# Kernel tuning notes

Hardware: AMD Instinct MI355X
Metric: run time of the kernel (lower is better)

The kernel has to match this reference:

```python
import jax, jax.numpy as jnp
import numpy as np

EMBED_DIM = 1024
NUM_HEADS = 16
HEAD_DIM = EMBED_DIM // NUM_HEADS


def setup_inputs() -> dict:
    key = jax.random.key(0)
    ks = jax.random.split(key, 9)
    s = 1.0 / np.sqrt(EMBED_DIM)
    X = jax.random.normal(ks[0], (4, 2048, EMBED_DIM), dtype=jnp.float32)
    # Linear weights stored as [in, out] for x @ W + b
    Wq = jax.random.uniform(ks[1], (EMBED_DIM, EMBED_DIM), jnp.float32, -s, s)
    bq = jax.random.uniform(ks[2], (EMBED_DIM,), jnp.float32, -s, s)
    Wk = jax.random.uniform(ks[3], (EMBED_DIM, EMBED_DIM), jnp.float32, -s, s)
    bk = jax.random.uniform(ks[4], (EMBED_DIM,), jnp.float32, -s, s)
    Wv = jax.random.uniform(ks[5], (EMBED_DIM, EMBED_DIM), jnp.float32, -s, s)
    bv = jax.random.uniform(ks[6], (EMBED_DIM,), jnp.float32, -s, s)
    Wo = jax.random.uniform(ks[7], (EMBED_DIM, EMBED_DIM), jnp.float32, -s, s)
    bo = jax.random.uniform(ks[8], (EMBED_DIM,), jnp.float32, -s, s)
    return {"X": X, "Wq": Wq, "bq": bq, "Wk": Wk, "bk": bk,
            "Wv": Wv, "bv": bv, "Wo": Wo, "bo": bo}


def reference(X, Wq, bq, Wk, bk, Wv, bv, Wo, bo):
    B, S, _ = X.shape
    def split_heads(t):  # [B,S,E] -> [B,H,S,D]
        return t.reshape(B, S, NUM_HEADS, HEAD_DIM).transpose(0, 2, 1, 3)
    Q = split_heads(X @ Wq + bq)
    K = split_heads(X @ Wk + bk)
    V = split_heads(X @ Wv + bv)
    scale = 1.0 / np.sqrt(HEAD_DIM).astype(np.float32)
    scores = jnp.einsum('bhqd,bhkd->bhqk', Q, K) * scale
    probs = jax.nn.softmax(scores, axis=-1)
    attn = jnp.einsum('bhqk,bhkd->bhqd', probs, V)  # [B,H,S,D]
    combined = attn.transpose(0, 2, 1, 3).reshape(B, S, EMBED_DIM)
    return combined @ Wo + bo
```

## Files before the change

kernel.cpp:

```cpp
#include <hip/hip_runtime.h>
#include <hip/hip_bf16.h>

#define EMBED 1024
#define NHEADS 16
#define HDIM 64
#define SEQ 2048
#define BATCH 4
#define ROWS (BATCH * SEQ)

typedef __attribute__((ext_vector_type(8))) short bf16x8;
typedef __attribute__((ext_vector_type(4))) float f32x4;
typedef __attribute__((ext_vector_type(2))) float f32x2;
typedef __attribute__((ext_vector_type(16))) float f32x16;
typedef __attribute__((ext_vector_type(4))) unsigned int u32x4;
typedef __attribute__((ext_vector_type(2))) unsigned int u32x2;
typedef __attribute__((ext_vector_type(2))) int i32x2;
typedef unsigned int u32;

#define SL2E 0.18033688011112042f

__device__ __forceinline__ short f2bf(float f) {
    u32 u = __builtin_bit_cast(u32, f) + 0x8000u;
    return (short)(u >> 16);
}

__device__ __forceinline__ u32 pkbf(float a, float b) {
    u32 ua = __builtin_bit_cast(u32, a) + 0x8000u;
    u32 ub = __builtin_bit_cast(u32, b) + 0x8000u;
    return __builtin_amdgcn_perm(ua, ub, 0x03020706u);
}

__device__ __forceinline__ u32 cvtpk(float a, float b) {
    u32 r;
    asm("v_cvt_pk_bf16_f32 %0, %1, %2" : "=v"(r) : "v"(a), "v"(b));
    return r;
}

__device__ __forceinline__ float fexp2(float x) {
#if __has_builtin(__builtin_amdgcn_exp2f)
    return __builtin_amdgcn_exp2f(x);
#else
    return exp2f(x);
#endif
}

__device__ __forceinline__ void async16(const void* g, void* l) {
    __builtin_amdgcn_global_load_lds((const __attribute__((address_space(1))) u32*)g,
                                     (__attribute__((address_space(3))) u32*)l, 16, 0, 0);
}

__global__ __launch_bounds__(256) void prep(const float* __restrict__ X,
                                            short* __restrict__ Xbf,
                                            const float* __restrict__ W0,
                                            const float* __restrict__ W1,
                                            const float* __restrict__ W2,
                                            const float* __restrict__ W3,
                                            short* __restrict__ T0,
                                            short* __restrict__ T1,
                                            short* __restrict__ T2,
                                            short* __restrict__ T3) {
    const int bid = blockIdx.x;
    if (bid < 8192) {
        int i = (bid * 256 + threadIdx.x) * 4;
        float4 v = *(const float4*)&X[i];
        u32x2 o = { pkbf(v.x, v.y), pkbf(v.z, v.w) };
        *(u32x2*)&Xbf[i] = o;
        return;
    }
    const int id = bid - 8192;
    const int z = id >> 8;
    const int rem = id & 255;
    const int n0 = (rem & 15) * 64, k0 = (rem >> 4) * 64;
    const float* W = (z == 0) ? W0 : (z == 1) ? W1 : (z == 2) ? W2 : W3;
    short* WT = (z == 0) ? T0 : (z == 1) ? T1 : (z == 2) ? T2 : T3;
    const float sc = (z == 0) ? SL2E : 1.0f;
    __shared__ float T[64][65];
    const int rr = threadIdx.x >> 4, cc = (threadIdx.x & 15) * 4;
    #pragma unroll
    for (int p = 0; p < 4; ++p) {
        int r = p * 16 + rr;
        float4 v = *(const float4*)&W[(size_t)(k0 + r) * EMBED + n0 + cc];
        T[r][cc] = v.x * sc; T[r][cc + 1] = v.y * sc; T[r][cc + 2] = v.z * sc; T[r][cc + 3] = v.w * sc;
    }
    __syncthreads();
    #pragma unroll
    for (int p = 0; p < 4; ++p) {
        int r = p * 16 + rr;
        u32x2 o = { pkbf(T[cc][r], T[cc + 1][r]), pkbf(T[cc + 2][r], T[cc + 3][r]) };
        *(u32x2*)&WT[(size_t)(n0 + r) * EMBED + k0 + cc] = o;
    }
}

__global__ __launch_bounds__(512, 2) void gemm_p128(const short* __restrict__ A,
                                                    const short* __restrict__ BT,
                                                    const float* __restrict__ b0,
                                                    const float* __restrict__ b1,
                                                    const float* __restrict__ b2,
                                                    void* __restrict__ C0,
                                                    void* __restrict__ C1,
                                                    void* __restrict__ C2,
                                                    int mode) {
    __shared__ short As[2][8192];
    __shared__ short Bs[2][16384];
    const int tid = threadIdx.x;
    const int lane = tid & 63;
    const int wid = tid >> 6;
    const int c16 = lane & 15, quad = lane >> 4, sw = c16 & 7;
    const int wm = wid >> 2, wn = wid & 3;
    const int gx = gridDim.x;
    const int hid = blockIdx.y * gx + blockIdx.x;
    const int cpx = (gx * gridDim.y) >> 3;
    const int tle = (hid & 7) * cpx + (hid >> 3);
    const int bx = tle % gx, by = tle / gx;
    const int rowblk = by * 128, colblk = bx * 256;

    const int r0 = tid >> 3;
    const int g0 = (tid & 7) ^ (r0 & 7);
    const short* aS0 = A + (size_t)(rowblk + r0) * EMBED + g0 * 8;
    const short* bS0 = BT + (size_t)(colblk + r0) * EMBED + g0 * 8;

#define STAGE_A(SBUF, V) do { \
    const short* _s = aS0 + (V) * 64; \
    async16(_s,         &As[SBUF][tid * 8]); \
    async16(_s + 65536, &As[SBUF][tid * 8 + 4096]); \
} while (0)
#define STAGE_B0(SBUF, V) do { \
    const short* _s = bS0 + (V) * 64; \
    async16(_s,         &Bs[SBUF][tid * 8]); \
    async16(_s + 65536, &Bs[SBUF][tid * 8 + 4096]); \
} while (0)
#define STAGE_B1(SBUF, V) do { \
    const short* _s = bS0 + 131072 + (V) * 64; \
    async16(_s,         &Bs[SBUF][tid * 8 + 8192]); \
    async16(_s + 65536, &Bs[SBUF][tid * 8 + 12288]); \
} while (0)

    f32x4 acc[4][4] = {};
    bf16x8 aU[2][2], bE[2][2], bO[2][2];

#define LDA(BUF, MH) do { \
    _Pragma("unroll") \
    for (int fm = 0; fm < 2; ++fm) { \
        const int row = wm * 64 + (MH) * 32 + fm * 16 + c16; \
        _Pragma("unroll") \
        for (int ks = 0; ks < 2; ++ks) \
            aU[fm][ks] = *(const bf16x8*)&As[BUF][row * 64 + ((ks * 4 + quad) ^ sw) * 8]; \
    } \
} while (0)
#define LDB(BUF, NH, DST) do { \
    _Pragma("unroll") \
    for (int fn = 0; fn < 2; ++fn) { \
        const int col = wn * 64 + (NH) * 32 + fn * 16 + c16; \
        _Pragma("unroll") \
        for (int ks = 0; ks < 2; ++ks) \
            DST[fn][ks] = *(const bf16x8*)&Bs[BUF][col * 64 + ((ks * 4 + quad) ^ sw) * 8]; \
    } \
} while (0)
#define MM(MB, NB, BM_) do { \
    _Pragma("unroll") \
    for (int fm = 0; fm < 2; ++fm) \
        _Pragma("unroll") \
        for (int fn = 0; fn < 2; ++fn) \
            _Pragma("unroll") \
            for (int ks = 0; ks < 2; ++ks) \
                acc[(MB) + fm][(NB) + fn] = \
                    __builtin_amdgcn_mfma_f32_16x16x32_bf16(aU[fm][ks], BM_[fn][ks], \
                        acc[(MB) + fm][(NB) + fn], 0, 0, 0); \
} while (0)
#define PH_MID() do { \
    __builtin_amdgcn_s_barrier(); \
    asm volatile("s_waitcnt lgkmcnt(0)" ::: "memory"); \
    __builtin_amdgcn_s_setprio(1); \
} while (0)
#define PH_END(VM) do { \
    __builtin_amdgcn_s_setprio(0); \
    if (VM) asm volatile("s_waitcnt vmcnt(6)" ::: "memory"); \
    __builtin_amdgcn_s_barrier(); \
} while (0)

    STAGE_B0(0, 0); STAGE_A(0, 0); STAGE_B1(0, 0);
    STAGE_B0(1, 1); STAGE_A(1, 1); STAGE_B1(1, 1);
    asm volatile("s_waitcnt vmcnt(6)" ::: "memory");
    __builtin_amdgcn_s_barrier();

    #pragma unroll 1
    for (int it = 0; it < 8; ++it) {
        const int u = 2 * it;
        const int v2 = (u + 2) & 15, v3 = (u + 3) & 15;
        LDA(0, 0); LDB(0, 0, bE);                     PH_MID(); MM(0, 0, bE); PH_END(0);
        LDB(0, 1, bO);            STAGE_B0(0, v2);    PH_MID(); MM(0, 2, bO); PH_END(0);
        LDA(0, 1);                STAGE_B1(0, v2);    PH_MID(); MM(2, 2, bO); PH_END(0);
                 STAGE_A(0, v2);     PH_MID(); MM(2, 0, bE); PH_END(1);
        LDA(1, 0); LDB(1, 0, bE);                     PH_MID(); MM(0, 0, bE); PH_END(0);
        LDB(1, 1, bO);            STAGE_B0(1, v3);    PH_MID(); MM(0, 2, bO); PH_END(0);
        LDA(1, 1);                STAGE_B1(1, v3);    PH_MID(); MM(2, 2, bO); PH_END(0);
                 STAGE_A(1, v3);     PH_MID(); MM(2, 0, bE); PH_END(1);
    }

    asm volatile("s_waitcnt vmcnt(0)" ::: "memory");

    const int rb0 = rowblk + wm * 64 + quad * 4;
    const int cb0 = wn * 64 + c16;
    if (mode == 0) {
        const int z = colblk >> 10;
        const int cm = colblk & 1023;
        const float* bias = (z == 0) ? b0 : (z == 1) ? b1 : b2;
        if (z == 2) {
            short* Vt = (short*)C2;
            #pragma unroll
            for (int m = 0; m < 4; ++m) {
                const int row = rb0 + (m >> 1) * 32 + (m & 1) * 16;
                const int b = row >> 11, s = row & 2047;
                #pragma unroll
                for (int n = 0; n < 4; ++n) {
                    const int cv = cm + cb0 + (n >> 1) * 32 + (n & 1) * 16;
                    const int head = cv >> 6, d = cv & 63;
                    const float bv = bias[cv];
                    u32x2 o = { pkbf(acc[m][n][0] + bv, acc[m][n][1] + bv),
                                pkbf(acc[m][n][2] + bv, acc[m][n][3] + bv) };
                    *(u32x2*)&Vt[((size_t)(b * NHEADS + head) * HDIM + d) * SEQ + s] = o;
                }
            }
        } else {
            short* Cq = (short*)((z == 0) ? C0 : C1);
            const float bsc = (z == 0) ? SL2E : 1.0f;
            #pragma unroll
            for (int m = 0; m < 4; ++m) {
                const int row = rb0 + (m >> 1) * 32 + (m & 1) * 16;
                #pragma unroll
                for (int n = 0; n < 4; ++n) {
                    const int col = cm + cb0 + (n >> 1) * 32 + (n & 1) * 16;
                    const float bv = bias[col] * bsc;
                    #pragma unroll
                    for (int r = 0; r < 4; ++r)
                        Cq[(size_t)(row + r) * EMBED + col] = f2bf(acc[m][n][r] + bv);
                }
            }
        }
    } else {
        float* Co = (float*)C0;
        #pragma unroll
        for (int m = 0; m < 4; ++m) {
            const int row = rb0 + (m >> 1) * 32 + (m & 1) * 16;
            #pragma unroll
            for (int n = 0; n < 4; ++n) {
                const int col = colblk + cb0 + (n >> 1) * 32 + (n & 1) * 16;
                const float bv = b0[col];
                #pragma unroll
                for (int r = 0; r < 4; ++r)
                    Co[(size_t)(row + r) * EMBED + col] = acc[m][n][r] + bv;
            }
        }
    }
#undef PH_END
#undef PH_MID
#undef MM
#undef LDB
#undef LDA
#undef STAGE_B1
#undef STAGE_B0
#undef STAGE_A
}

__global__ __launch_bounds__(512, 2) void gemm_k64(const short* __restrict__ A,
                                                   const short* __restrict__ BT,
                                                   const float* __restrict__ bias,
                                                   float* __restrict__ C) {
    __shared__ short As[2][8192];
    __shared__ short Bs[2][8192];
    const int tid = threadIdx.x;
    const int lane = tid & 63, wid = tid >> 6;
    const int c16 = lane & 15, quad = lane >> 4, sw = c16 & 7;
    const int wm = wid >> 2, wn = wid & 3;
    const int gx = gridDim.x;
    const int hid = blockIdx.y * gx + blockIdx.x;
    const int cpx = (gx * gridDim.y) >> 3;
    const int tle = (hid & 7) * cpx + (hid >> 3);
    const int bx = tle % gx, by = tle / gx;
    const int rowblk = by * 128, colblk = bx * 128;

    const int r0 = tid >> 3;
    const int g0 = (tid & 7) ^ (r0 & 7);
    const short* aS = A + (size_t)(rowblk + r0) * EMBED + g0 * 8;
    const short* bS = BT + (size_t)(colblk + r0) * EMBED + g0 * 8;

#define STG(SBUF, V) do { \
    const short* _a = aS + (V) * 64; \
    const short* _b = bS + (V) * 64; \
    async16(_a,         &As[SBUF][tid * 8]); \
    async16(_a + 65536, &As[SBUF][tid * 8 + 4096]); \
    async16(_b,         &Bs[SBUF][tid * 8]); \
    async16(_b + 65536, &Bs[SBUF][tid * 8 + 4096]); \
} while (0)

    f32x4 acc[4][2] = {};

    STG(0, 0);
    asm volatile("s_waitcnt vmcnt(0)" ::: "memory");
    __builtin_amdgcn_s_barrier();

    #pragma unroll 2
    for (int t = 0; t < 16; ++t) {
        const int cur = t & 1;
        if (t < 15) STG(cur ^ 1, t + 1);
        bf16x8 af[4][2], bfv[2][2];
        #pragma unroll
        for (int fm = 0; fm < 4; ++fm) {
            const int row = wm * 64 + fm * 16 + c16;
            #pragma unroll
            for (int ks = 0; ks < 2; ++ks)
                af[fm][ks] = *(const bf16x8*)&As[cur][row * 64 + ((ks * 4 + quad) ^ sw) * 8];
        }
        #pragma unroll
        for (int fn = 0; fn < 2; ++fn) {
            const int col = wn * 32 + fn * 16 + c16;
            #pragma unroll
            for (int ks = 0; ks < 2; ++ks)
                bfv[fn][ks] = *(const bf16x8*)&Bs[cur][col * 64 + ((ks * 4 + quad) ^ sw) * 8];
        }
        __builtin_amdgcn_s_setprio(1);
        #pragma unroll
        for (int fm = 0; fm < 4; ++fm)
            #pragma unroll
            for (int fn = 0; fn < 2; ++fn)
                #pragma unroll
                for (int ks = 0; ks < 2; ++ks)
                    acc[fm][fn] = __builtin_amdgcn_mfma_f32_16x16x32_bf16(af[fm][ks], bfv[fn][ks], acc[fm][fn], 0, 0, 0);
        __builtin_amdgcn_s_setprio(0);
        asm volatile("s_waitcnt vmcnt(0)" ::: "memory");
        __builtin_amdgcn_s_barrier();
    }

    const int rb0 = rowblk + wm * 64 + quad * 4;
    const int cb0 = colblk + wn * 32 + c16;
    #pragma unroll
    for (int fm = 0; fm < 4; ++fm) {
        const int row = rb0 + fm * 16;
        #pragma unroll
        for (int fn = 0; fn < 2; ++fn) {
            const int col = cb0 + fn * 16;
            const float bv = bias[col];
            #pragma unroll
            for (int r = 0; r < 4; ++r)
                C[(size_t)(row + r) * EMBED + col] = acc[fm][fn][r] + bv;
        }
    }
#undef STG
}

__global__ __launch_bounds__(256, 4) void attn_mfma(const short* __restrict__ Qb,
                                                    const short* __restrict__ Kb,
                                                    const short* __restrict__ Vt,
                                                    short* __restrict__ Ob) {
    __shared__ short SH[16384];
    const int tid = threadIdx.x;
    const int wave = tid >> 6, lane = tid & 63;
    const int l31 = lane & 31, h = lane >> 5;
    const int swz = l31 & 7;
    const int hid = blockIdx.y * 16 + blockIdx.x;
    const int tle = (hid & 7) * 128 + (hid >> 3);
    const int qb = tle & 15, bh = tle >> 4;
    const int b = bh >> 4, hd = bh & 15;
    const size_t base = (size_t)b * SEQ * EMBED + (size_t)hd * HDIM;
    const size_t vbase = (size_t)bh * HDIM * SEQ;
    const int q0 = qb * 128;

    bf16x8 qf[4];
    #pragma unroll
    for (int ks = 0; ks < 4; ++ks)
        qf[ks] = *(const bf16x8*)&Qb[base + (size_t)(q0 + wave * 32 + l31) * EMBED + ks * 16 + h * 8];

    const short* kp[2];
    const short* vp[2];
    int ldofs[2];
    #pragma unroll
    for (int it = 0; it < 2; ++it) {
        int ci = (it * 4 + wave) * 64 + lane;
        int row = ci >> 3, g = (ci & 7) ^ (row & 7);
        kp[it] = Kb + base + (size_t)row * EMBED + g * 8;
        vp[it] = Vt + vbase + (size_t)row * SEQ + g * 8;
        ldofs[it] = (it * 4 + wave) * 512;
    }

#define STAGE_KV(J) do { \
    async16(kp[0], &SH[(J) * 4096 + ldofs[0]]); \
    async16(kp[1], &SH[(J) * 4096 + ldofs[1]]); \
    async16(vp[0], &SH[8192 + (J) * 4096 + ldofs[0]]); \
    async16(vp[1], &SH[8192 + (J) * 4096 + ldofs[1]]); \
    kp[0] += 64 * EMBED; kp[1] += 64 * EMBED; \
    vp[0] += 64; vp[1] += 64; \
} while (0)

    f32x16 O[2] = {};
    f32x2 ls = {0.0f, 0.0f};

    STAGE_KV(0);
    asm volatile("s_waitcnt vmcnt(0)" ::: "memory");
    __builtin_amdgcn_s_barrier();

#define ATT_TILE(CUR, NXT, DO_STAGE) do { \
    if (DO_STAGE) STAGE_KV(NXT); \
    _Pragma("unroll") \
    for (int nt = 0; nt < 2; ++nt) { \
        f32x16 st = {0.0f, 0.0f, 0.0f, 0.0f, 0.0f, 0.0f, 0.0f, 0.0f, \
                     0.0f, 0.0f, 0.0f, 0.0f, 0.0f, 0.0f, 0.0f, 0.0f}; \
        __builtin_amdgcn_s_setprio(1); \
        _Pragma("unroll") \
        for (int ks = 0; ks < 4; ++ks) { \
            bf16x8 ak = *(const bf16x8*)&SH[(CUR) * 4096 + (nt * 32 + l31) * 64 + ((ks * 2 + h) ^ swz) * 8]; \
            st = __builtin_amdgcn_mfma_f32_32x32x16_bf16(ak, qf[ks], st, 0, 0, 0); \
        } \
        __builtin_amdgcn_s_setprio(0); \
        u32 pk[8]; \
        _Pragma("unroll") \
        for (int i = 0; i < 8; ++i) { \
            float e0 = fexp2(st[2 * i]), e1 = fexp2(st[2 * i + 1]); \
            f32x2 e = { e0, e1 }; \
            ls += e; \
            pk[i] = cvtpk(e0, e1); \
        } \
        __builtin_amdgcn_s_setprio(1); \
        _Pragma("unroll") \
        for (int kk = 0; kk < 2; ++kk) { \
            const int ks = nt * 2 + kk, bs = kk * 4; \
            u32x4 fr; \
            i32x2 sA = __builtin_amdgcn_permlane32_swap((int)pk[bs + 0], (int)pk[bs + 2], false, false); \
            i32x2 sB = __builtin_amdgcn_permlane32_swap((int)pk[bs + 1], (int)pk[bs + 3], false, false); \
            fr.x = (u32)sA.x; fr.y = (u32)sB.x; fr.z = (u32)sA.y; fr.w = (u32)sB.y; \
            bf16x8 pf = __builtin_bit_cast(bf16x8, fr); \
            _Pragma("unroll") \
            for (int mt = 0; mt < 2; ++mt) { \
                bf16x8 vf = *(const bf16x8*)&SH[8192 + (CUR) * 4096 + (mt * 32 + l31) * 64 + ((ks * 2 + h) ^ swz) * 8]; \
                O[mt] = __builtin_amdgcn_mfma_f32_32x32x16_bf16(vf, pf, O[mt], 0, 0, 0); \
            } \
        } \
        __builtin_amdgcn_s_setprio(0); \
    } \
    asm volatile("s_waitcnt vmcnt(0)" ::: "memory"); \
    __builtin_amdgcn_s_barrier(); \
} while (0)

    #pragma unroll 1
    for (int t = 0; t < 30; t += 2) {
        ATT_TILE(0, 1, 1);
        ATT_TILE(1, 0, 1);
    }
    ATT_TILE(0, 1, 1);
    ATT_TILE(1, 0, 0);

#undef ATT_TILE
#undef STAGE_KV

    float lsum = ls.x + ls.y;
    lsum += __shfl_xor(lsum, 32);
    float inv = 1.0f / lsum;

    const int wbase = wave * 2048;
    #pragma unroll
    for (int mt = 0; mt < 2; ++mt)
        #pragma unroll
        for (int m = 0; m < 4; ++m) {
            u32x2 wv;
            wv.x = pkbf(O[mt][4 * m + 0] * inv, O[mt][4 * m + 1] * inv);
            wv.y = pkbf(O[mt][4 * m + 2] * inv, O[mt][4 * m + 3] * inv);
            int u = mt * 8 + 2 * m + h;
            int su = u ^ ((l31 & 7) << 1);
            *(u32x2*)&SH[wbase + l31 * 64 + su * 4] = wv;
        }
    __syncthreads();
    #pragma unroll
    for (int p = 0; p < 4; ++p) {
        int ci = p * 256 + tid;
        int wq = ci >> 8, rem = ci & 255;
        int r = rem >> 3, cch = rem & 7;
        int su = (2 * cch) ^ ((r & 7) << 1);
        bf16x8 val = *(const bf16x8*)&SH[wq * 2048 + r * 64 + su * 4];
        *(bf16x8*)&Ob[base + (size_t)(q0 + wq * 32 + r) * EMBED + cch * 8] = val;
    }
}

extern "C" void kernel_launch(void* const* d_in, const int* in_sizes, int n_in,
                              void* d_out, int out_size, void* d_ws, size_t ws_size,
                              hipStream_t stream)
{
    const float* X  = (const float*)d_in[0];
    const float* Wq = (const float*)d_in[1];
    const float* bq = (const float*)d_in[2];
    const float* Wk = (const float*)d_in[3];
    const float* bk = (const float*)d_in[4];
    const float* Wv = (const float*)d_in[5];
    const float* bv = (const float*)d_in[6];
    const float* Wo = (const float*)d_in[7];
    const float* bo = (const float*)d_in[8];
    float* out = (float*)d_out;

    const size_t NE = (size_t)ROWS * EMBED;
    short* Xbf = (short*)d_ws;
    short* Qb  = Xbf + NE;
    short* Kb  = Qb + NE;
    short* Vtb = Kb + NE;
    short* WqT = Vtb + NE;
    short* WkT = WqT + (size_t)EMBED * EMBED;
    short* WvT = WkT + (size_t)EMBED * EMBED;
    short* WoT = WvT + (size_t)EMBED * EMBED;

    prep<<<9216, 256, 0, stream>>>(X, Xbf, Wq, Wk, Wv, Wo, WqT, WkT, WvT, WoT);

    dim3 gq(12, 64, 1);
    gemm_p128<<<gq, 512, 0, stream>>>(Xbf, WqT, bq, bk, bv, Qb, Kb, Vtb, 0);

    dim3 gt(SEQ / 128, BATCH * NHEADS);
    attn_mfma<<<gt, 256, 0, stream>>>(Qb, Kb, Vtb, Qb);

    dim3 gg(8, 64, 1);
    gemm_k64<<<gg, 512, 0, stream>>>(Qb, WoT, bo, out);
}
```

Measured before the change: 255.9 us.

## Replace 128x256 ping-pong QKV GEMM with simpler 128x128 double-buffered kernel

The QKV projection GEMM moves from a 128x256 tile with a phased ping-pong schedule (barriers, priority toggling, partial vmcnt waits) to a 128x128 tile with a plain double-buffered loop. It also launches twice as many blocks and halves the shared-memory B buffer. The aim is better occupancy, a simpler schedule and less barrier overhead. The trade-offs are lower arithmetic intensity per tile, more redundant A loads, and a full vmcnt(0) wait every K step, which removes the fine-grained overlap.

```diff
diff --git a/kernel.cpp b/kernel.cpp
--- a/kernel.cpp
+++ b/kernel.cpp
@@ -91,20 +91,18 @@
     }
 }
 
-__global__ __launch_bounds__(512, 2) void gemm_p128(const short* __restrict__ A,
-                                                    const short* __restrict__ BT,
-                                                    const float* __restrict__ b0,
-                                                    const float* __restrict__ b1,
-                                                    const float* __restrict__ b2,
-                                                    void* __restrict__ C0,
-                                                    void* __restrict__ C1,
-                                                    void* __restrict__ C2,
-                                                    int mode) {
+__global__ __launch_bounds__(512, 2) void gemm_qkv128(const short* __restrict__ A,
+                                                      const short* __restrict__ BT,
+                                                      const float* __restrict__ b0,
+                                                      const float* __restrict__ b1,
+                                                      const float* __restrict__ b2,
+                                                      short* __restrict__ Cq,
+                                                      short* __restrict__ Ck,
+                                                      short* __restrict__ Vt) {
     __shared__ short As[2][8192];
-    __shared__ short Bs[2][16384];
+    __shared__ short Bs[2][8192];
     const int tid = threadIdx.x;
-    const int lane = tid & 63;
-    const int wid = tid >> 6;
+    const int lane = tid & 63, wid = tid >> 6;
     const int c16 = lane & 15, quad = lane >> 4, sw = c16 & 7;
     const int wm = wid >> 2, wn = wid & 3;
     const int gx = gridDim.x;
@@ -112,154 +110,97 @@
     const int cpx = (gx * gridDim.y) >> 3;
     const int tle = (hid & 7) * cpx + (hid >> 3);
     const int bx = tle % gx, by = tle / gx;
-    const int rowblk = by * 128, colblk = bx * 256;
+    const int rowblk = by * 128, colblk = bx * 128;
 
     const int r0 = tid >> 3;
     const int g0 = (tid & 7) ^ (r0 & 7);
-    const short* aS0 = A + (size_t)(rowblk + r0) * EMBED + g0 * 8;
-    const short* bS0 = BT + (size_t)(colblk + r0) * EMBED + g0 * 8;
-
-#define STAGE_A(SBUF, V) do { \
-    const short* _s = aS0 + (V) * 64; \
-    async16(_s,         &As[SBUF][tid * 8]); \
-    async16(_s + 65536, &As[SBUF][tid * 8 + 4096]); \
+    const short* aS = A + (size_t)(rowblk + r0) * EMBED + g0 * 8;
+    const short* bS = BT + (size_t)(colblk + r0) * EMBED + g0 * 8;
+
+#define STG(SBUF, V) do { \
+    const short* _a = aS + (V) * 64; \
+    const short* _b = bS + (V) * 64; \
+    async16(_a,         &As[SBUF][tid * 8]); \
+    async16(_a + 65536, &As[SBUF][tid * 8 + 4096]); \
+    async16(_b,         &Bs[SBUF][tid * 8]); \
+    async16(_b + 65536, &Bs[SBUF][tid * 8 + 4096]); \
 } while (0)
-#define STAGE_B0(SBUF, V) do { \
-    const short* _s = bS0 + (V) * 64; \
-    async16(_s,         &Bs[SBUF][tid * 8]); \
-    async16(_s + 65536, &Bs[SBUF][tid * 8 + 4096]); \
-} while (0)
-#define STAGE_B1(SBUF, V) do { \
-    const short* _s = bS0 + 131072 + (V) * 64; \
-    async16(_s,         &Bs[SBUF][tid * 8 + 8192]); \
-    async16(_s + 65536, &Bs[SBUF][tid * 8 + 12288]); \
-} while (0)
-
-    f32x4 acc[4][4] = {};
-    bf16x8 aU[2][2], bE[2][2], bO[2][2];
-
-#define LDA(BUF, MH) do { \
-    _Pragma("unroll") \
-    for (int fm = 0; fm < 2; ++fm) { \
-        const int row = wm * 64 + (MH) * 32 + fm * 16 + c16; \
-        _Pragma("unroll") \
-        for (int ks = 0; ks < 2; ++ks) \
-            aU[fm][ks] = *(const bf16x8*)&As[BUF][row * 64 + ((ks * 4 + quad) ^ sw) * 8]; \
-    } \
-} while (0)
-#define LDB(BUF, NH, DST) do { \
-    _Pragma("unroll") \
-    for (int fn = 0; fn < 2; ++fn) { \
-        const int col = wn * 64 + (NH) * 32 + fn * 16 + c16; \
-        _Pragma("unroll") \
-        for (int ks = 0; ks < 2; ++ks) \
-            DST[fn][ks] = *(const bf16x8*)&Bs[BUF][col * 64 + ((ks * 4 + quad) ^ sw) * 8]; \
-    } \
-} while (0)
-#define MM(MB, NB, BM_) do { \
-    _Pragma("unroll") \
-    for (int fm = 0; fm < 2; ++fm) \
-        _Pragma("unroll") \
-        for (int fn = 0; fn < 2; ++fn) \
-            _Pragma("unroll") \
-            for (int ks = 0; ks < 2; ++ks) \
-                acc[(MB) + fm][(NB) + fn] = \
-                    __builtin_amdgcn_mfma_f32_16x16x32_bf16(aU[fm][ks], BM_[fn][ks], \
-                        acc[(MB) + fm][(NB) + fn], 0, 0, 0); \
-} while (0)
-#define PH_MID() do { \
-    __builtin_amdgcn_s_barrier(); \
-    asm volatile("s_waitcnt lgkmcnt(0)" ::: "memory"); \
-    __builtin_amdgcn_s_setprio(1); \
-} while (0)
-#define PH_END(VM) do { \
-    __builtin_amdgcn_s_setprio(0); \
-    if (VM) asm volatile("s_waitcnt vmcnt(6)" ::: "memory"); \
-    __builtin_amdgcn_s_barrier(); \
-} while (0)
-
-    STAGE_B0(0, 0); STAGE_A(0, 0); STAGE_B1(0, 0);
-    STAGE_B0(1, 1); STAGE_A(1, 1); STAGE_B1(1, 1);
-    asm volatile("s_waitcnt vmcnt(6)" ::: "memory");
+
+    f32x4 acc[4][2] = {};
+
+    STG(0, 0);
+    asm volatile("s_waitcnt vmcnt(0)" ::: "memory");
     __builtin_amdgcn_s_barrier();
 
-    #pragma unroll 1
-    for (int it = 0; it < 8; ++it) {
-        const int u = 2 * it;
-        const int v2 = (u + 2) & 15, v3 = (u + 3) & 15;
-        LDA(0, 0); LDB(0, 0, bE);                     PH_MID(); MM(0, 0, bE); PH_END(0);
-        LDB(0, 1, bO);            STAGE_B0(0, v2);    PH_MID(); MM(0, 2, bO); PH_END(0);
-        LDA(0, 1);                STAGE_B1(0, v2);    PH_MID(); MM(2, 2, bO); PH_END(0);
-                 STAGE_A(0, v2);     PH_MID(); MM(2, 0, bE); PH_END(1);
-        LDA(1, 0); LDB(1, 0, bE);                     PH_MID(); MM(0, 0, bE); PH_END(0);
-        LDB(1, 1, bO);            STAGE_B0(1, v3);    PH_MID(); MM(0, 2, bO); PH_END(0);
-        LDA(1, 1);                STAGE_B1(1, v3);    PH_MID(); MM(2, 2, bO); PH_END(0);
-                 STAGE_A(1, v3);     PH_MID(); MM(2, 0, bE); PH_END(1);
-    }
-
-    asm volatile("s_waitcnt vmcnt(0)" ::: "memory");
+    #pragma unroll 2
+    for (int t = 0; t < 16; ++t) {
+        const int cur = t & 1;
+        if (t < 15) STG(cur ^ 1, t + 1);
+        bf16x8 af[4][2], bfv[2][2];
+        #pragma unroll
+        for (int fm = 0; fm < 4; ++fm) {
+            const int row = wm * 64 + fm * 16 + c16;
+            #pragma unroll
+            for (int ks = 0; ks < 2; ++ks)
+                af[fm][ks] = *(const bf16x8*)&As[cur][row * 64 + ((ks * 4 + quad) ^ sw) * 8];
+        }
+        #pragma unroll
+        for (int fn = 0; fn < 2; ++fn) {
+            const int col = wn * 32 + fn * 16 + c16;
+            #pragma unroll
+            for (int ks = 0; ks < 2; ++ks)
+                bfv[fn][ks] = *(const bf16x8*)&Bs[cur][col * 64 + ((ks * 4 + quad) ^ sw) * 8];
+        }
+        __builtin_amdgcn_s_setprio(1);
+        #pragma unroll
+        for (int fm = 0; fm < 4; ++fm)
+            #pragma unroll
+            for (int fn = 0; fn < 2; ++fn)
+                #pragma unroll
+                for (int ks = 0; ks < 2; ++ks)
+                    acc[fm][fn] = __builtin_amdgcn_mfma_f32_16x16x32_bf16(af[fm][ks], bfv[fn][ks], acc[fm][fn], 0, 0, 0);
+        __builtin_amdgcn_s_setprio(0);
+        asm volatile("s_waitcnt vmcnt(0)" ::: "memory");
+        __builtin_amdgcn_s_barrier();
+    }
 
     const int rb0 = rowblk + wm * 64 + quad * 4;
-    const int cb0 = wn * 64 + c16;
-    if (mode == 0) {
-        const int z = colblk >> 10;
-        const int cm = colblk & 1023;
-        const float* bias = (z == 0) ? b0 : (z == 1) ? b1 : b2;
-        if (z == 2) {
-            short* Vt = (short*)C2;
-            #pragma unroll
-            for (int m = 0; m < 4; ++m) {
-                const int row = rb0 + (m >> 1) * 32 + (m & 1) * 16;
-                const int b = row >> 11, s = row & 2047;
-                #pragma unroll
-                for (int n = 0; n < 4; ++n) {
-                    const int cv = cm + cb0 + (n >> 1) * 32 + (n & 1) * 16;
-                    const int head = cv >> 6, d = cv & 63;
-                    const float bv = bias[cv];
-                    u32x2 o = { pkbf(acc[m][n][0] + bv, acc[m][n][1] + bv),
-                                pkbf(acc[m][n][2] + bv, acc[m][n][3] + bv) };
-                    *(u32x2*)&Vt[((size_t)(b * NHEADS + head) * HDIM + d) * SEQ + s] = o;
-                }
+    const int z = colblk >> 10;
+    const int cm = colblk & 1023;
+    const int cb0 = cm + wn * 32 + c16;
+    const float* bias = (z == 0) ? b0 : (z == 1) ? b1 : b2;
+    if (z == 2) {
+        #pragma unroll
+        for (int fm = 0; fm < 4; ++fm) {
+            const int row = rb0 + fm * 16;
+            const int b = row >> 11, s = row & 2047;
+            #pragma unroll
+            for (int fn = 0; fn < 2; ++fn) {
+                const int cv = cb0 + fn * 16;
+                const int head = cv >> 6, d = cv & 63;
+                const float bv = bias[cv];
+                u32x2 o = { pkbf(acc[fm][fn][0] + bv, acc[fm][fn][1] + bv),
+                            pkbf(acc[fm][fn][2] + bv, acc[fm][fn][3] + bv) };
+                *(u32x2*)&Vt[((size_t)(b * NHEADS + head) * HDIM + d) * SEQ + s] = o;
             }
-        } else {
-            short* Cq = (short*)((z == 0) ? C0 : C1);
-            const float bsc = (z == 0) ? SL2E : 1.0f;
-            #pragma unroll
-            for (int m = 0; m < 4; ++m) {
-                const int row = rb0 + (m >> 1) * 32 + (m & 1) * 16;
-                #pragma unroll
-                for (int n = 0; n < 4; ++n) {
-                    const int col = cm + cb0 + (n >> 1) * 32 + (n & 1) * 16;
-                    const float bv = bias[col] * bsc;
-                    #pragma unroll
-                    for (int r = 0; r < 4; ++r)
-                        Cq[(size_t)(row + r) * EMBED + col] = f2bf(acc[m][n][r] + bv);
-                }
-            }
         }
     } else {
-        float* Co = (float*)C0;
-        #pragma unroll
-        for (int m = 0; m < 4; ++m) {
-            const int row = rb0 + (m >> 1) * 32 + (m & 1) * 16;
-            #pragma unroll
-            for (int n = 0; n < 4; ++n) {
-                const int col = colblk + cb0 + (n >> 1) * 32 + (n & 1) * 16;
-                const float bv = b0[col];
+        short* Cout = (z == 0) ? Cq : Ck;
+        const float bsc = (z == 0) ? SL2E : 1.0f;
+        #pragma unroll
+        for (int fm = 0; fm < 4; ++fm) {
+            const int row = rb0 + fm * 16;
+            #pragma unroll
+            for (int fn = 0; fn < 2; ++fn) {
+                const int col = cb0 + fn * 16;
+                const float bv = bias[col] * bsc;
                 #pragma unroll
                 for (int r = 0; r < 4; ++r)
-                    Co[(size_t)(row + r) * EMBED + col] = acc[m][n][r] + bv;
+                    Cout[(size_t)(row + r) * EMBED + col] = f2bf(acc[fm][fn][r] + bv);
             }
         }
     }
-#undef PH_END
-#undef PH_MID
-#undef MM
-#undef LDB
-#undef LDA
-#undef STAGE_B1
-#undef STAGE_B0
-#undef STAGE_A
+#undef STG
 }
 
 __global__ __launch_bounds__(512, 2) void gemm_k64(const short* __restrict__ A,
@@ -506,8 +447,8 @@
 
     prep<<<9216, 256, 0, stream>>>(X, Xbf, Wq, Wk, Wv, Wo, WqT, WkT, WvT, WoT);
 
-    dim3 gq(12, 64, 1);
-    gemm_p128<<<gq, 512, 0, stream>>>(Xbf, WqT, bq, bk, bv, Qb, Kb, Vtb, 0);
+    dim3 gq(24, 64, 1);
+    gemm_qkv128<<<gq, 512, 0, stream>>>(Xbf, WqT, bq, bk, bv, Qb, Kb, Vtb);
 
     dim3 gt(SEQ / 128, BATCH * NHEADS);
     attn_mfma<<<gt, 256, 0, stream>>>(Qb, Kb, Vtb, Qb);
```

Result: no change. 254.0 us, median of 2 (-0.8%).
